# Kernel optimization log

Hardware: AMD Instinct MI355X
Metric: run time of the kernel (lower is better)

The kernel has to match this reference:

```python
import jax, jax.numpy as jnp
import numpy as np

D_MODEL = 1024
NUM_HEADS = 16
HEAD_DIM = D_MODEL // NUM_HEADS


def setup_inputs() -> dict:
    key = jax.random.key(0)
    kx, kq, kk, kv, ko = jax.random.split(key, 5)
    init_std = float(np.sqrt(2.0 / (D_MODEL + D_MODEL)))
    def trunc(k):
        # trunc normal in [-3std, 3std], matching nn.init.trunc_normal_
        return jax.random.truncated_normal(k, -3.0, 3.0, (D_MODEL, D_MODEL), jnp.float32) * init_std
    return {
        "x": jax.random.normal(kx, (2, 2048, D_MODEL), jnp.float32),
        "Wq": trunc(kq),
        "Wk": trunc(kk),
        "Wv": trunc(kv),
        "Wo": trunc(ko),
    }


def reference(x, Wq, Wk, Wv, Wo):
    b, s, _ = x.shape
    # projections: Linear computes x @ W.T with W [out, in]
    q = (x @ Wq.T).reshape(b, s, NUM_HEADS, HEAD_DIM).transpose(0, 2, 1, 3)
    k = (x @ Wk.T).reshape(b, s, NUM_HEADS, HEAD_DIM).transpose(0, 2, 1, 3)
    v = (x @ Wv.T).reshape(b, s, NUM_HEADS, HEAD_DIM).transpose(0, 2, 1, 3)
    scale = 1.0 / jnp.sqrt(jnp.float32(HEAD_DIM))
    logits = jnp.einsum("bhqd,bhkd->bhqk", q, k)  # [b,h,s,s]
    causal = jnp.tril(jnp.ones((s, s), dtype=bool))
    logits = jnp.where(causal, logits, -jnp.inf)
    attn = jax.nn.softmax(logits * scale, axis=-1)
    out = jnp.einsum("bhqk,bhkd->bhqd", attn, v)
    out = out.transpose(0, 2, 1, 3).reshape(b, s, D_MODEL)
    return out @ Wo.T
```

## Files before the change

### kernel.cpp

```cpp
#include <hip/hip_runtime.h>
#include <hip/hip_bf16.h>


#define DEVI __device__ __forceinline__

typedef __bf16 bf16x8 __attribute__((ext_vector_type(8)));
typedef short  short8 __attribute__((ext_vector_type(8)));
typedef float  f32x4  __attribute__((ext_vector_type(4)));
typedef float  f32x16 __attribute__((ext_vector_type(16)));
typedef unsigned int u32x4 __attribute__((ext_vector_type(4)));

DEVI short f2bfs(float f) {
    __hip_bfloat16 h = __float2bfloat16(f);
    return __builtin_bit_cast(short, h);
}
DEVI unsigned pack2(float a, float b) {
    return (unsigned)(unsigned short)f2bfs(a) | ((unsigned)(unsigned short)f2bfs(b) << 16);
}
DEVI bf16x8 ld8(const short* p) {
    return __builtin_bit_cast(bf16x8, *(const short8*)p);
}
DEVI void gload16(const void* g, void* lds) {
    __builtin_amdgcn_global_load_lds(
        (const __attribute__((address_space(1))) void*)g,
        (__attribute__((address_space(3))) void*)lds, 16, 0, 0);
}
DEVI void plswap(unsigned& a, unsigned& b) {
    asm volatile("v_permlane32_swap_b32 %0, %1" : "+v"(a), "+v"(b));
}
DEVI const short* lds_swc(const short* base, int row, int col) {
    return (const short*)((const char*)base + (((row << 7) + (col << 1)) ^ ((row & 7) << 4)));
}

#if defined(__has_builtin)
#if __has_builtin(__builtin_amdgcn_exp2f)
#define HAVE_EXP2 1
#endif
#endif
DEVI float ex2(float x) {
#ifdef HAVE_EXP2
    return __builtin_amdgcn_exp2f(x);
#else
    return __expf(x * 0.69314718055994531f);
#endif
}
#define CEXP 0.18033688011112042f

__global__ __launch_bounds__(256) void convert_kernel(
    const float* __restrict__ x, const float* __restrict__ Wq,
    const float* __restrict__ Wk, const float* __restrict__ Wv,
    const float* __restrict__ Wo, short* __restrict__ xb, short* __restrict__ wb) {
    const int bid = blockIdx.x;
    const float* src;
    short* dst;
    int i8;
    if (bid < 2048) {
        src = x; dst = xb;
        i8 = (bid * 256 + threadIdx.x) * 8;
    } else {
        const int w = bid - 2048;
        const int z = w >> 9;
        src = (z == 0) ? Wq : (z == 1) ? Wk : (z == 2) ? Wv : Wo;
        dst = wb + (size_t)z * 1048576;
        i8 = (((w & 511) * 256) + threadIdx.x) * 8;
    }
    float4 a = ((const float4*)(src + i8))[0];
    float4 b = ((const float4*)(src + i8))[1];
    short8 t;
    t[0] = f2bfs(a.x); t[1] = f2bfs(a.y); t[2] = f2bfs(a.z); t[3] = f2bfs(a.w);
    t[4] = f2bfs(b.x); t[5] = f2bfs(b.y); t[6] = f2bfs(b.z); t[7] = f2bfs(b.w);
    *(short8*)(dst + i8) = t;
}

template <int BM, int BN, int MF, int NF, int WN>
DEVI void gemm_kloop64(const short* __restrict__ A, const short* __restrict__ B,
                       short* As, short* Bs, int wid, int lane, f32x4 acc[MF][NF]) {
    const int l15 = lane & 15, l4 = lane >> 4;
    const int wm = wid / WN, wn = wid % WN;
    const int rowc = lane >> 3;
    const int gcol = ((lane & 7) ^ rowc) * 8;
    constexpr int NCHA = BM / 8, NCHB = BN / 8;
#pragma unroll 1
    for (int k0 = 0; k0 < 1024; k0 += 64) {
        __syncthreads();
#pragma unroll
        for (int c = wid; c < NCHA; c += 4)
            gload16(A + (size_t)(c * 8 + rowc) * 1024 + k0 + gcol, As + c * 512);
#pragma unroll
        for (int c = wid; c < NCHB; c += 4)
            gload16(B + (size_t)(c * 8 + rowc) * 1024 + k0 + gcol, Bs + c * 512);
        __syncthreads();
#pragma unroll
        for (int kk = 0; kk < 2; ++kk) {
            bf16x8 af[MF], bf[NF];
#pragma unroll
            for (int m = 0; m < MF; ++m) {
                const int row = wm * (MF * 16) + m * 16 + l15;
                af[m] = ld8(As + row * 64 + (((kk * 4 + l4) ^ (row & 7)) * 8));
            }
#pragma unroll
            for (int n = 0; n < NF; ++n) {
                const int row = wn * (NF * 16) + n * 16 + l15;
                bf[n] = ld8(Bs + row * 64 + (((kk * 4 + l4) ^ (row & 7)) * 8));
            }
#pragma unroll
            for (int m = 0; m < MF; ++m)
#pragma unroll
                for (int n = 0; n < NF; ++n)
                    acc[m][n] = __builtin_amdgcn_mfma_f32_16x16x32_bf16(af[m], bf[n], acc[m][n], 0, 0, 0);
        }
    }
}

__global__ __launch_bounds__(256) void gemm_qkv_kernel(
    const short* __restrict__ xb, const short* __restrict__ wb,
    short* __restrict__ Qo, short* __restrict__ Ko, short* __restrict__ VtG) {
    __shared__ short As[8192], Bs[8192];
    const int tid = threadIdx.x, lane = tid & 63, wid = tid >> 6;
    const int l15 = lane & 15, l4 = lane >> 4;
    const int wm = wid >> 1, wn = wid & 1;
    const int y = blockIdx.y, wsel = y >> 3;
    const int row0 = blockIdx.x * 128, col0 = (y & 7) * 128;

    f32x4 acc[4][4] = {};
    gemm_kloop64<128, 128, 4, 4, 2>(
        xb + (size_t)row0 * 1024,
        wb + (size_t)wsel * 1048576 + (size_t)col0 * 1024,
        As, Bs, wid, lane, acc);

    if (wsel == 2) {
#pragma unroll
        for (int m = 0; m < 4; ++m)
#pragma unroll
            for (int n = 0; n < 4; ++n)
#pragma unroll
                for (int j = 0; j < 4; ++j) {
                    int row = row0 + wm * 64 + m * 16 + l4 * 4 + j;
                    int col = col0 + wn * 64 + n * 16 + l15;
                    VtG[(size_t)col * 4096 + row] = f2bfs(acc[m][n][j]);
                }
    } else {
        short* C = (wsel == 0) ? Qo : Ko;
#pragma unroll
        for (int m = 0; m < 4; ++m)
#pragma unroll
            for (int n = 0; n < 4; ++n)
#pragma unroll
                for (int j = 0; j < 4; ++j) {
                    int row = row0 + wm * 64 + m * 16 + l4 * 4 + j;
                    int col = col0 + wn * 64 + n * 16 + l15;
                    C[(size_t)row * 1024 + col] = f2bfs(acc[m][n][j]);
                }
    }
}

__global__ __launch_bounds__(256) void gemm_wo_kernel(
    const short* __restrict__ Ao, const short* __restrict__ Wob,
    float* __restrict__ Cout) {
    __shared__ short As[4096], Bs[8192];
    const int tid = threadIdx.x, lane = tid & 63, wid = tid >> 6;
    const int l15 = lane & 15, l4 = lane >> 4;
    const int wn = wid;
    const int row0 = blockIdx.x * 64, col0 = blockIdx.y * 128;

    f32x4 acc[4][2] = {};
    gemm_kloop64<64, 128, 4, 2, 4>(
        Ao + (size_t)row0 * 1024, Wob + (size_t)col0 * 1024,
        As, Bs, wid, lane, acc);

#pragma unroll
    for (int m = 0; m < 4; ++m)
#pragma unroll
        for (int n = 0; n < 2; ++n)
#pragma unroll
            for (int j = 0; j < 4; ++j) {
                int row = row0 + m * 16 + l4 * 4 + j;
                int col = col0 + wn * 32 + n * 16 + l15;
                Cout[(size_t)row * 1024 + col] = acc[m][n][j];
            }
}

DEVI void attn_tile(int kv0, bool diag, const short* Ks, const short* Vts,
                    const bf16x8 qf[4], f32x16& o0, f32x16& o1,
                    float& m, float& l, int qrow, int l31, int hi) {
    f32x16 s0 = 0.0f, s1 = 0.0f;
    __builtin_amdgcn_s_setprio(1);
#pragma unroll
    for (int ds = 0; ds < 4; ++ds) {
        bf16x8 kf = ld8(lds_swc(Ks, l31, ds * 16 + hi * 8));
        s0 = __builtin_amdgcn_mfma_f32_32x32x16_bf16(kf, qf[ds], s0, 0, 0, 0);
    }
#pragma unroll
    for (int ds = 0; ds < 4; ++ds) {
        bf16x8 kf = ld8(lds_swc(Ks, 32 + l31, ds * 16 + hi * 8));
        s1 = __builtin_amdgcn_mfma_f32_32x32x16_bf16(kf, qf[ds], s1, 0, 0, 0);
    }
    __builtin_amdgcn_s_setprio(0);

    if (diag) {
#pragma unroll
        for (int r = 0; r < 16; ++r) {
            const int kvr = kv0 + (r & 3) + 8 * (r >> 2) + 4 * hi;
            if (kvr > qrow)      s0[r] = -3.0e38f;
            if (kvr + 32 > qrow) s1[r] = -3.0e38f;
        }
    }
    float mx0 = -3.0e38f, mx1 = -3.0e38f, mx2 = -3.0e38f, mx3 = -3.0e38f;
#pragma unroll
    for (int r = 0; r < 16; r += 4) {
        mx0 = fmaxf(mx0, fmaxf(s0[r],     s1[r]));
        mx1 = fmaxf(mx1, fmaxf(s0[r + 1], s1[r + 1]));
        mx2 = fmaxf(mx2, fmaxf(s0[r + 2], s1[r + 2]));
        mx3 = fmaxf(mx3, fmaxf(s0[r + 3], s1[r + 3]));
    }
    float pmax = fmaxf(fmaxf(mx0, mx1), fmaxf(mx2, mx3));
    pmax = fmaxf(pmax, __shfl_xor(pmax, 32, 64));

    if (__any(pmax > m + 64.0f)) {
        const float mnew = fmaxf(m, pmax);
        const float corr = ex2((m - mnew) * CEXP);
        m = mnew;
        l *= corr;
#pragma unroll
        for (int r = 0; r < 16; ++r) {
            const int cr = (r & 3) + 8 * (r >> 2) + 4 * hi;
            const float c = __shfl(corr, cr, 64);
            o0[r] *= c; o1[r] *= c;
        }
    }

    const float mc = m * CEXP;
    float r0 = 0.f, r1 = 0.f, r2 = 0.f, r3 = 0.f;
    unsigned w0[8], w1[8];
#pragma unroll
    for (int i = 0; i < 8; ++i) {
        const float p0 = ex2(__builtin_fmaf(s0[2 * i],     CEXP, -mc));
        const float p1 = ex2(__builtin_fmaf(s0[2 * i + 1], CEXP, -mc));
        const float p2 = ex2(__builtin_fmaf(s1[2 * i],     CEXP, -mc));
        const float p3 = ex2(__builtin_fmaf(s1[2 * i + 1], CEXP, -mc));
        r0 += p0; r1 += p1; r2 += p2; r3 += p3;
        w0[i] = pack2(p0, p1);
        w1[i] = pack2(p2, p3);
    }
    const float rsum = (r0 + r1) + (r2 + r3);
    l += rsum + __shfl_xor(rsum, 32, 64);

    __builtin_amdgcn_s_setprio(1);
#pragma unroll
    for (int c = 0; c < 2; ++c) {
        const unsigned* w = (c == 0) ? w0 : w1;
        unsigned a0 = w[0], a2 = w[2]; plswap(a0, a2);
        unsigned a1 = w[1], a3 = w[3]; plswap(a1, a3);
        unsigned a4 = w[4], a6 = w[6]; plswap(a4, a6);
        unsigned a5 = w[5], a7 = w[7]; plswap(a5, a7);
        u32x4 lo, hw;
        lo[0] = a0; lo[1] = a1; lo[2] = a2; lo[3] = a3;
        hw[0] = a4; hw[1] = a5; hw[2] = a6; hw[3] = a7;
        const bf16x8 paL = __builtin_bit_cast(bf16x8, lo);
        const bf16x8 paH = __builtin_bit_cast(bf16x8, hw);

        bf16x8 vb;
        vb = ld8(lds_swc(Vts, l31,      c * 32 + hi * 8));
        o0 = __builtin_amdgcn_mfma_f32_32x32x16_bf16(paL, vb, o0, 0, 0, 0);
        vb = ld8(lds_swc(Vts, 32 + l31, c * 32 + hi * 8));
        o1 = __builtin_amdgcn_mfma_f32_32x32x16_bf16(paL, vb, o1, 0, 0, 0);
        vb = ld8(lds_swc(Vts, l31,      c * 32 + 16 + hi * 8));
        o0 = __builtin_amdgcn_mfma_f32_32x32x16_bf16(paH, vb, o0, 0, 0, 0);
        vb = ld8(lds_swc(Vts, 32 + l31, c * 32 + 16 + hi * 8));
        o1 = __builtin_amdgcn_mfma_f32_32x32x16_bf16(paH, vb, o1, 0, 0, 0);
    }
    __builtin_amdgcn_s_setprio(0);
}

__global__ __launch_bounds__(128) void attn_kernel(
    const short* __restrict__ Q, const short* __restrict__ K,
    const short* __restrict__ VtG, short* __restrict__ O) {
    __shared__ short KsA[4096], VtsA[4096], KsB[4096], VtsB[4096];

    const int tid = threadIdx.x, lane = tid & 63, wid = tid >> 6;
    const int l31 = lane & 31, hi = lane >> 5;
    const int bid = blockIdx.x;
    const int qt = 31 - (bid >> 5);
    const int bh = bid & 31;
    const int b = bh >> 4, h = bh & 15;
    const size_t base = (size_t)b * 2048 * 1024 + (size_t)h * 64;
    const short* Qp = Q + base;
    const short* Kp = K + base;
    const short* Vp = VtG + (size_t)(h * 64) * 4096 + (size_t)b * 2048;
    short* Op = O + base;

    const int q0w = qt * 64 + wid * 32;
    const int qrow = q0w + l31;

    const int srw = lane >> 3;
    const int swc = ((lane & 7) ^ srw) * 8;
    const short* kSrc = Kp + (size_t)srw * 1024 + swc;
    const short* vSrc = Vp + (size_t)srw * 4096 + swc;
    const int cc0 = wid * 4;

#define ISSUE_TILE(Ksb, Vtsb, kv0_)                                           \
    {                                                                         \
        const int kv0i = (kv0_);                                              \
        _Pragma("unroll")                                                     \
        for (int c = 0; c < 4; ++c) {                                         \
            const int cc = cc0 + c;                                           \
            gload16(kSrc + (size_t)(kv0i + cc * 8) * 1024, (Ksb) + cc * 512); \
            gload16(vSrc + (size_t)(cc * 8) * 4096 + kv0i, (Vtsb) + cc * 512);\
        }                                                                     \
    }

    ISSUE_TILE(KsA, VtsA, 0);

    bf16x8 qf[4];
#pragma unroll
    for (int ds = 0; ds < 4; ++ds)
        qf[ds] = ld8(Qp + (size_t)qrow * 1024 + ds * 16 + hi * 8);

    f32x16 o0 = 0.0f, o1 = 0.0f;
    float m = -INFINITY, l = 0.0f;
    const int ntiles = qt + 1;

#pragma unroll 1
    for (int t = 0; t < ntiles; ++t) {
        const short* Ks  = (t & 1) ? KsB  : KsA;
        const short* Vts = (t & 1) ? VtsB : VtsA;
        if (t + 1 < ntiles) {
            short* Ksn  = (t & 1) ? KsA  : KsB;
            short* Vtsn = (t & 1) ? VtsA : VtsB;
            ISSUE_TILE(Ksn, Vtsn, (t + 1) * 64);
            asm volatile("s_waitcnt vmcnt(8)" ::: "memory");
        } else {
            asm volatile("s_waitcnt vmcnt(0)" ::: "memory");
        }
        __builtin_amdgcn_s_barrier();
        __builtin_amdgcn_sched_barrier(0);
        attn_tile(t * 64, (t * 64 + 63 > q0w), Ks, Vts, qf, o0, o1, m, l, qrow, l31, hi);
        __builtin_amdgcn_s_barrier();
    }
#undef ISSUE_TILE

    const float il = 1.0f / l;
#pragma unroll
    for (int r = 0; r < 16; ++r) {
        const int cr = (r & 3) + 8 * (r >> 2) + 4 * hi;
        const float s = __shfl(il, cr, 64);
        const size_t row = (size_t)(q0w + cr) * 1024;
        Op[row + l31]      = f2bfs(o0[r] * s);
        Op[row + 32 + l31] = f2bfs(o1[r] * s);
    }
}

extern "C" void kernel_launch(void* const* d_in, const int* in_sizes, int n_in,
                              void* d_out, int out_size, void* d_ws, size_t ws_size,
                              hipStream_t stream) {
    const float* x  = (const float*)d_in[0];
    const float* Wq = (const float*)d_in[1];
    const float* Wk = (const float*)d_in[2];
    const float* Wv = (const float*)d_in[3];
    const float* Wo = (const float*)d_in[4];

    short* wb  = (short*)d_ws;
    short* Qw  = wb + (size_t)4 * 1048576;
    short* Kw  = Qw + (size_t)4194304;
    short* Vtw = Kw + (size_t)4194304;
    short* xb  = (short*)d_out;

    convert_kernel<<<4096, 256, 0, stream>>>(x, Wq, Wk, Wv, Wo, xb, wb);
    gemm_qkv_kernel<<<dim3(32, 24), 256, 0, stream>>>(xb, wb, Qw, Kw, Vtw);
    attn_kernel<<<1024, 128, 0, stream>>>(Qw, Kw, Vtw, Qw);
    gemm_wo_kernel<<<dim3(64, 8), 256, 0, stream>>>(Qw, wb + (size_t)3 * 1048576, (float*)d_out);
}
```

Measured before the change: 123.0 us.

## Prefetch K/V fragments into registers and peel diagonal tile in attention

The attention loop now reads all K and V fragments for a tile from LDS into registers before compute, and issues the next global-to-LDS load only after those reads finish. This lets one barrier per iteration suffice and gives the global loads a full tile of compute to hide behind. The causal-mask branch becomes a template parameter, and only the last tile runs the masked path. It raises register pressure by sixteen bf16x8 fragments and waits on vmcnt(0) each iteration, which may stall if loads are slow.

```diff
diff --git a/kernel.cpp b/kernel.cpp
--- a/kernel.cpp
+++ b/kernel.cpp
@@ -180,24 +180,37 @@
             }
 }
 
-DEVI void attn_tile(int kv0, bool diag, const short* Ks, const short* Vts,
-                    const bf16x8 qf[4], f32x16& o0, f32x16& o1,
-                    float& m, float& l, int qrow, int l31, int hi) {
+DEVI void read_frags(const short* Ks, const short* Vts, int l31, int hi,
+                     bf16x8 kf[8], bf16x8 vb[8]) {
+#pragma unroll
+    for (int ds = 0; ds < 4; ++ds) {
+        kf[ds]     = ld8(lds_swc(Ks, l31,      ds * 16 + hi * 8));
+        kf[4 + ds] = ld8(lds_swc(Ks, 32 + l31, ds * 16 + hi * 8));
+    }
+#pragma unroll
+    for (int c = 0; c < 2; ++c) {
+        vb[c * 4 + 0] = ld8(lds_swc(Vts, l31,      c * 32 + hi * 8));
+        vb[c * 4 + 1] = ld8(lds_swc(Vts, 32 + l31, c * 32 + hi * 8));
+        vb[c * 4 + 2] = ld8(lds_swc(Vts, l31,      c * 32 + 16 + hi * 8));
+        vb[c * 4 + 3] = ld8(lds_swc(Vts, 32 + l31, c * 32 + 16 + hi * 8));
+    }
+}
+
+template <bool DIAG>
+DEVI void attn_tile_r(int kv0, const bf16x8 kf[8], const bf16x8 vb[8],
+                      const bf16x8 qf[4], f32x16& o0, f32x16& o1,
+                      float& m, float& l, int qrow, int hi) {
     f32x16 s0 = 0.0f, s1 = 0.0f;
     __builtin_amdgcn_s_setprio(1);
 #pragma unroll
-    for (int ds = 0; ds < 4; ++ds) {
-        bf16x8 kf = ld8(lds_swc(Ks, l31, ds * 16 + hi * 8));
-        s0 = __builtin_amdgcn_mfma_f32_32x32x16_bf16(kf, qf[ds], s0, 0, 0, 0);
-    }
-#pragma unroll
-    for (int ds = 0; ds < 4; ++ds) {
-        bf16x8 kf = ld8(lds_swc(Ks, 32 + l31, ds * 16 + hi * 8));
-        s1 = __builtin_amdgcn_mfma_f32_32x32x16_bf16(kf, qf[ds], s1, 0, 0, 0);
-    }
+    for (int ds = 0; ds < 4; ++ds)
+        s0 = __builtin_amdgcn_mfma_f32_32x32x16_bf16(kf[ds], qf[ds], s0, 0, 0, 0);
+#pragma unroll
+    for (int ds = 0; ds < 4; ++ds)
+        s1 = __builtin_amdgcn_mfma_f32_32x32x16_bf16(kf[4 + ds], qf[ds], s1, 0, 0, 0);
     __builtin_amdgcn_s_setprio(0);
 
-    if (diag) {
+    if (DIAG) {
 #pragma unroll
         for (int r = 0; r < 16; ++r) {
             const int kvr = kv0 + (r & 3) + 8 * (r >> 2) + 4 * hi;
@@ -259,15 +272,10 @@
         const bf16x8 paL = __builtin_bit_cast(bf16x8, lo);
         const bf16x8 paH = __builtin_bit_cast(bf16x8, hw);
 
-        bf16x8 vb;
-        vb = ld8(lds_swc(Vts, l31,      c * 32 + hi * 8));
-        o0 = __builtin_amdgcn_mfma_f32_32x32x16_bf16(paL, vb, o0, 0, 0, 0);
-        vb = ld8(lds_swc(Vts, 32 + l31, c * 32 + hi * 8));
-        o1 = __builtin_amdgcn_mfma_f32_32x32x16_bf16(paL, vb, o1, 0, 0, 0);
-        vb = ld8(lds_swc(Vts, l31,      c * 32 + 16 + hi * 8));
-        o0 = __builtin_amdgcn_mfma_f32_32x32x16_bf16(paH, vb, o0, 0, 0, 0);
-        vb = ld8(lds_swc(Vts, 32 + l31, c * 32 + 16 + hi * 8));
-        o1 = __builtin_amdgcn_mfma_f32_32x32x16_bf16(paH, vb, o1, 0, 0, 0);
+        o0 = __builtin_amdgcn_mfma_f32_32x32x16_bf16(paL, vb[c * 4 + 0], o0, 0, 0, 0);
+        o1 = __builtin_amdgcn_mfma_f32_32x32x16_bf16(paL, vb[c * 4 + 1], o1, 0, 0, 0);
+        o0 = __builtin_amdgcn_mfma_f32_32x32x16_bf16(paH, vb[c * 4 + 2], o0, 0, 0, 0);
+        o1 = __builtin_amdgcn_mfma_f32_32x32x16_bf16(paH, vb[c * 4 + 3], o1, 0, 0, 0);
     }
     __builtin_amdgcn_s_setprio(0);
 }
@@ -309,6 +317,8 @@
         }                                                                     \
     }
 
+    const int nt = qt + 1;
+
     ISSUE_TILE(KsA, VtsA, 0);
 
     bf16x8 qf[4];
@@ -316,27 +326,36 @@
     for (int ds = 0; ds < 4; ++ds)
         qf[ds] = ld8(Qp + (size_t)qrow * 1024 + ds * 16 + hi * 8);
 
+    asm volatile("s_waitcnt vmcnt(0)" ::: "memory");
+    __builtin_amdgcn_s_barrier();
+    __builtin_amdgcn_sched_barrier(0);
+
+    bf16x8 kf[8], vb[8];
+    read_frags(KsA, VtsA, l31, hi, kf, vb);
+    __builtin_amdgcn_sched_barrier(0);
+    if (nt > 1) ISSUE_TILE(KsB, VtsB, 64);
+
     f32x16 o0 = 0.0f, o1 = 0.0f;
     float m = -INFINITY, l = 0.0f;
-    const int ntiles = qt + 1;
 
 #pragma unroll 1
-    for (int t = 0; t < ntiles; ++t) {
-        const short* Ks  = (t & 1) ? KsB  : KsA;
-        const short* Vts = (t & 1) ? VtsB : VtsA;
-        if (t + 1 < ntiles) {
-            short* Ksn  = (t & 1) ? KsA  : KsB;
-            short* Vtsn = (t & 1) ? VtsA : VtsB;
-            ISSUE_TILE(Ksn, Vtsn, (t + 1) * 64);
-            asm volatile("s_waitcnt vmcnt(8)" ::: "memory");
-        } else {
-            asm volatile("s_waitcnt vmcnt(0)" ::: "memory");
-        }
+    for (int t = 0; t < nt - 1; ++t) {
+        attn_tile_r<false>(t * 64, kf, vb, qf, o0, o1, m, l, qrow, hi);
+        asm volatile("s_waitcnt lgkmcnt(0) vmcnt(0)" ::: "memory");
         __builtin_amdgcn_s_barrier();
         __builtin_amdgcn_sched_barrier(0);
-        attn_tile(t * 64, (t * 64 + 63 > q0w), Ks, Vts, qf, o0, o1, m, l, qrow, l31, hi);
-        __builtin_amdgcn_s_barrier();
-    }
+        const short* Ksn  = (t & 1) ? KsA  : KsB;
+        const short* Vtsn = (t & 1) ? VtsA : VtsB;
+        read_frags(Ksn, Vtsn, l31, hi, kf, vb);
+        __builtin_amdgcn_sched_barrier(0);
+        if (t + 2 < nt) {
+            short* Kso  = (t & 1) ? KsB  : KsA;
+            short* Vtso = (t & 1) ? VtsB : VtsA;
+            ISSUE_TILE(Kso, Vtso, (t + 2) * 64);
+        }
+    }
+
+    attn_tile_r<true>((nt - 1) * 64, kf, vb, qf, o0, o1, m, l, qrow, hi);
 #undef ISSUE_TILE
 
     const float il = 1.0f / l;
```

Result: faster. 120.3 us (-2.2%).
